# Optimization experiments

Measured on AMD Instinct MI355X. Metric: run time of the kernel, lower is better.

## Reference

```python
import jax, jax.numpy as jnp
import numpy as np

BATCH, T, N = 64, 512, 1024

def setup_inputs() -> dict:
    key = jax.random.key(0)
    k1, k2, k3 = jax.random.split(key, 3)
    input_sequence = jax.random.normal(k1, (BATCH, T, N), dtype=jnp.float32)
    W_self_lower = jax.random.normal(k2, (N, N), dtype=jnp.float32) * 0.1
    W_input = jax.random.normal(k3, (N, N), dtype=jnp.float32) * 0.1
    return {"input_sequence": input_sequence, "W_self_lower": W_self_lower, "W_input": W_input}

def reference(input_sequence, W_self_lower, W_input):
    # W_self symmetric: (W + W.T)/2; note W_self.T == W_self
    W_self = (W_self_lower + W_self_lower.T) * 0.5
    batch = input_sequence.shape[0]
    n = W_self.shape[0]
    # Precompute input projection for all timesteps: (B, T, N) @ (N, N)^T
    x_proj = jnp.einsum('btn,mn->btm', input_sequence, W_input)
    h0 = jnp.zeros((batch, n), dtype=input_sequence.dtype)

    def step(h, xp_t):
        h_new = jnp.tanh(h @ W_self.T + xp_t)
        return h_new, h_new

    # scan over time axis: move T to leading axis
    _, states = jax.lax.scan(step, h0, jnp.swapaxes(x_proj, 0, 1))
    return jnp.swapaxes(states, 0, 1)  # (B, T, N)
```

## Files before the change

### kernel.cpp

```cpp
#include <hip/hip_runtime.h>
#include <cstdint>
#include <cmath>

constexpr int BATCH = 64;
constexpr int T     = 512;
constexpr int N     = 1024;
constexpr int NWG   = 256;
constexpr int NG    = 32;
constexpr int GM    = 16;

typedef float f4 __attribute__((ext_vector_type(4)));
typedef short s4 __attribute__((ext_vector_type(4)));
typedef short bs8 __attribute__((ext_vector_type(8)));

struct alignas(128) PadInt { int v; int pad[31]; };
__device__ PadInt g_cnt[NG];
__device__ PadInt g_flag[NG];

__device__ __forceinline__ f4 ld_sys_x4(const float* p) {
  f4 v;
  asm volatile("global_load_dwordx4 %0, %1, off sc0 sc1" : "=v"(v) : "v"(p));
  return v;
}
__device__ __forceinline__ int ld_sys_i32(const int* p) {
  int v;
  asm volatile("global_load_dword %0, %1, off sc0 sc1\n\ts_waitcnt vmcnt(0)"
               : "=v"(v) : "v"(p) : "memory");
  return v;
}
__device__ __forceinline__ void st_sys_f32(float* p, float v) {
  asm volatile("global_store_dword %0, %1, off sc0 sc1 nt" ::"v"(p), "v"(v)
               : "memory");
}
__device__ __forceinline__ void wait_vm0(void) {
  asm volatile("s_waitcnt vmcnt(0)" ::: "memory");
  __builtin_amdgcn_sched_barrier(0);
}

__device__ __forceinline__ void arrive_cnt(int g, int t) {
  int old = __hip_atomic_fetch_add(&g_cnt[g].v, 1, __ATOMIC_RELAXED,
                                   __HIP_MEMORY_SCOPE_AGENT);
  if (old == t * GM + (GM - 1))
    __hip_atomic_store(&g_flag[g].v, t + 1, __ATOMIC_RELAXED,
                       __HIP_MEMORY_SCOPE_AGENT);
}
__device__ __forceinline__ void pollf(int g, int e) {
  while (ld_sys_i32(&g_flag[g].v) < e) __builtin_amdgcn_s_sleep(1);
}

__device__ __forceinline__ unsigned short f2bf(float f) {
  unsigned u = __builtin_bit_cast(unsigned, f);
  u = u + 0x7FFFu + ((u >> 16) & 1u);
  return (unsigned short)(u >> 16);
}
__device__ __forceinline__ float bf2f(unsigned short b) {
  unsigned u = ((unsigned)b) << 16;
  return __builtin_bit_cast(float, u);
}
__device__ __forceinline__ void mk8hilo(const float* p, bs8& hi, bs8& lo) {
  f4 a = *reinterpret_cast<const f4*>(p);
  f4 b = *reinterpret_cast<const f4*>(p + 4);
  float v[8] = {a[0], a[1], a[2], a[3], b[0], b[1], b[2], b[3]};
#pragma unroll
  for (int j = 0; j < 8; ++j) {
    unsigned short h = f2bf(v[j]);
    hi[j] = (short)h;
    lo[j] = (short)f2bf(v[j] - bf2f(h));
  }
}

__global__ __launch_bounds__(256) void symm_k(const float* __restrict__ W,
                                              float* __restrict__ Ws) {
  if (blockIdx.x == 0 && blockIdx.y == 0 && threadIdx.x < NG) {
    __hip_atomic_store(&g_cnt[threadIdx.x].v, 0, __ATOMIC_RELAXED,
                       __HIP_MEMORY_SCOPE_AGENT);
    __hip_atomic_store(&g_flag[threadIdx.x].v, 0, __ATOMIC_RELAXED,
                       __HIP_MEMORY_SCOPE_AGENT);
  }
  int j = blockIdx.x * 16 + (threadIdx.x & 15);
  int i = blockIdx.y * 16 + (threadIdx.x >> 4);
  Ws[(size_t)i * N + j] = 0.5f * (W[(size_t)i * N + j] + W[(size_t)j * N + i]);
}

__global__ __launch_bounds__(256) void xproj_gemm(const float* __restrict__ A,
                                                  const float* __restrict__ B,
                                                  float* __restrict__ C,
                                                  int M) {
  constexpr int BM = 128, BN = 128, BK = 16;
  __shared__ float As[BK][BM + 4];
  __shared__ float Bs[BK][BN + 4];

  const int tid = threadIdx.x;
  const int lin = blockIdx.x + gridDim.x * blockIdx.y;
  const int sw  = ((lin & 7) << 8) + (lin >> 3);
  const int bm  = sw >> 3;
  const int bn  = sw & 7;
  const int tx = tid & 15, ty = tid >> 4;
  const int K = N;

  float acc[8][8];
#pragma unroll
  for (int i = 0; i < 8; ++i)
#pragma unroll
    for (int j = 0; j < 8; ++j) acc[i][j] = 0.f;

  for (int kt = 0; kt < K; kt += BK) {
#pragma unroll
    for (int s = 0; s < 2; ++s) {
      int f = tid + s * 256;
      int row = f >> 2, kq = f & 3;
      float4 a = *reinterpret_cast<const float4*>(
          &A[(size_t)(bm * BM + row) * K + kt + kq * 4]);
      As[kq * 4 + 0][row] = a.x;
      As[kq * 4 + 1][row] = a.y;
      As[kq * 4 + 2][row] = a.z;
      As[kq * 4 + 3][row] = a.w;
      float4 b = *reinterpret_cast<const float4*>(
          &B[(size_t)(bn * BN + row) * K + kt + kq * 4]);
      Bs[kq * 4 + 0][row] = b.x;
      Bs[kq * 4 + 1][row] = b.y;
      Bs[kq * 4 + 2][row] = b.z;
      Bs[kq * 4 + 3][row] = b.w;
    }
    __syncthreads();

#pragma unroll
    for (int k = 0; k < BK; ++k) {
      float a[8], b[8];
      *reinterpret_cast<float4*>(&a[0]) =
          *reinterpret_cast<const float4*>(&As[k][ty * 8]);
      *reinterpret_cast<float4*>(&a[4]) =
          *reinterpret_cast<const float4*>(&As[k][ty * 8 + 4]);
      *reinterpret_cast<float4*>(&b[0]) =
          *reinterpret_cast<const float4*>(&Bs[k][tx * 8]);
      *reinterpret_cast<float4*>(&b[4]) =
          *reinterpret_cast<const float4*>(&Bs[k][tx * 8 + 4]);
#pragma unroll
      for (int i = 0; i < 8; ++i)
#pragma unroll
        for (int j = 0; j < 8; ++j) acc[i][j] = fmaf(a[i], b[j], acc[i][j]);
    }
    __syncthreads();
  }

#pragma unroll
  for (int i = 0; i < 8; ++i) {
    size_t row = (size_t)bm * BM + ty * 8 + i;
#pragma unroll
    for (int j = 0; j < 8; j += 4) {
      *reinterpret_cast<float4*>(&C[row * N + bn * BN + tx * 8 + j]) =
          *reinterpret_cast<const float4*>(&acc[i][j]);
    }
  }
}

__global__ __launch_bounds__(640, 1) void rnn_persist(
    float* __restrict__ out, const float* __restrict__ Ws) {
  const int tid = threadIdx.x;
  const int wg  = blockIdx.x;
  const int p   = wg & 15;
  const int cg  = wg >> 4;
  const int m0  = cg * 64;
  const int gA  = 2 * p, gB = 2 * p + 1;
  const int b0A = gA * 2, b0B = gB * 2;
  const size_t TN = (size_t)T * N;

  __shared__ __align__(16) short wloF[65536];
  __shared__ __align__(16) short hsA[4][1032];
  __shared__ __align__(16) short hsB[4][1032];
  __shared__ float xplA[128], xplB[128];
  __shared__ float redA[8 * 128], redB[8 * 128];
  __shared__ int lflags[64];

  if (tid == 0) {
    lflags[0] = -1; lflags[16] = -1;
    lflags[8] = 0;  lflags[24] = 0;
    lflags[32] = 0; lflags[48] = 0;
  }

  const int l = tid & 63;
  const int v = tid >> 6;
  const int n = l & 15;
  const int g = l >> 4;

  bs8 whi[4][4];
  if (v < 8) {
#pragma unroll
    for (int mt = 0; mt < 4; ++mt)
#pragma unroll
      for (int kt = 0; kt < 4; ++kt) {
        bs8 hi, lo;
        mk8hilo(&Ws[(size_t)(m0 + 16 * mt + n) * N + 128 * v + 32 * kt + 8 * g],
                hi, lo);
        whi[mt][kt] = hi;
        *reinterpret_cast<bs8*>(
            &wloF[((((v * 4 + mt) * 4 + kt) * 4 + g) * 16 + n) * 8]) = lo;
      }
  }
  __syncthreads();

  if (v < 8) {
    const int koff = 128 * v + 8 * g;
    const int hrow = n & 1;
    const int rcol = 8 * v + (l & 7);
    const int rnb  = (l >> 3) & 1;

    auto do_chain = [&](short (*hsX)[1032], float* xplX, float* redX,
                        int rdyIdx, int wsIdx, int ackIdx, int b0, int t) {
      while (*(volatile int*)&lflags[rdyIdx] < t) __builtin_amdgcn_s_sleep(1);
      __builtin_amdgcn_fence(__ATOMIC_ACQUIRE, "workgroup");
      if (t > 0) {
        f4 acc0 = {0.f, 0.f, 0.f, 0.f}, acc1 = {0.f, 0.f, 0.f, 0.f};
        f4 acc2 = {0.f, 0.f, 0.f, 0.f}, acc3 = {0.f, 0.f, 0.f, 0.f};
#pragma unroll
        for (int kt = 0; kt < 4; ++kt) {
          bs8 bhi = *reinterpret_cast<const bs8*>(&hsX[hrow][koff + 32 * kt]);
          bs8 blo = *reinterpret_cast<const bs8*>(&hsX[2 + hrow][koff + 32 * kt]);
          bs8 wl0 = *reinterpret_cast<const bs8*>(
              &wloF[((((v * 4 + 0) * 4 + kt) * 4 + g) * 16 + n) * 8]);
          bs8 wl1 = *reinterpret_cast<const bs8*>(
              &wloF[((((v * 4 + 1) * 4 + kt) * 4 + g) * 16 + n) * 8]);
          bs8 wl2 = *reinterpret_cast<const bs8*>(
              &wloF[((((v * 4 + 2) * 4 + kt) * 4 + g) * 16 + n) * 8]);
          bs8 wl3 = *reinterpret_cast<const bs8*>(
              &wloF[((((v * 4 + 3) * 4 + kt) * 4 + g) * 16 + n) * 8]);
          acc0 = __builtin_amdgcn_mfma_f32_16x16x32_bf16(whi[0][kt], bhi, acc0, 0, 0, 0);
          acc0 = __builtin_amdgcn_mfma_f32_16x16x32_bf16(whi[0][kt], blo, acc0, 0, 0, 0);
          acc0 = __builtin_amdgcn_mfma_f32_16x16x32_bf16(wl0, bhi, acc0, 0, 0, 0);
          acc1 = __builtin_amdgcn_mfma_f32_16x16x32_bf16(whi[1][kt], bhi, acc1, 0, 0, 0);
          acc1 = __builtin_amdgcn_mfma_f32_16x16x32_bf16(whi[1][kt], blo, acc1, 0, 0, 0);
          acc1 = __builtin_amdgcn_mfma_f32_16x16x32_bf16(wl1, bhi, acc1, 0, 0, 0);
          acc2 = __builtin_amdgcn_mfma_f32_16x16x32_bf16(whi[2][kt], bhi, acc2, 0, 0, 0);
          acc2 = __builtin_amdgcn_mfma_f32_16x16x32_bf16(whi[2][kt], blo, acc2, 0, 0, 0);
          acc2 = __builtin_amdgcn_mfma_f32_16x16x32_bf16(wl2, bhi, acc2, 0, 0, 0);
          acc3 = __builtin_amdgcn_mfma_f32_16x16x32_bf16(whi[3][kt], bhi, acc3, 0, 0, 0);
          acc3 = __builtin_amdgcn_mfma_f32_16x16x32_bf16(whi[3][kt], blo, acc3, 0, 0, 0);
          acc3 = __builtin_amdgcn_mfma_f32_16x16x32_bf16(wl3, bhi, acc3, 0, 0, 0);
        }
        if (n < 2) {
          const int rb = 4 * g;
#pragma unroll
          for (int r = 0; r < 4; ++r) {
            redX[v * 128 + (0  + rb + r) * 2 + n] = acc0[r];
            redX[v * 128 + (16 + rb + r) * 2 + n] = acc1[r];
            redX[v * 128 + (32 + rb + r) * 2 + n] = acc2[r];
            redX[v * 128 + (48 + rb + r) * 2 + n] = acc3[r];
          }
        }
      }
      __builtin_amdgcn_fence(__ATOMIC_RELEASE, "workgroup");
      if (l == 0) atomicAdd(&lflags[wsIdx], 1);
      while (*(volatile int*)&lflags[wsIdx] < 8 * (t + 1))
        __builtin_amdgcn_s_sleep(1);
      __builtin_amdgcn_fence(__ATOMIC_ACQUIRE, "workgroup");
      if (l < 16) {
        float pre = 0.f;
        if (t > 0) {
#pragma unroll
          for (int w = 0; w < 8; ++w)
            pre += redX[w * 128 + rcol * 2 + rnb];
        }
        float h = tanhf(pre + xplX[rnb * 64 + rcol]);
        st_sys_f32(out + (size_t)(b0 + rnb) * TN + (size_t)t * N + m0 + rcol,
                   h);
      }
      wait_vm0();
      if (l == 0) atomicAdd(&lflags[ackIdx], 1);
    };

    for (int t = 0; t < T; ++t) {
      do_chain(hsA, xplA, redA, 0, 8, 32, b0A, t);
      do_chain(hsB, xplB, redB, 16, 24, 48, b0B, t);
    }
  } else {
    const bool isB = (v == 9);
    const int lane = l;
    const int grp  = isB ? gB : gA;
    const int b0   = isB ? b0B : b0A;
    short (*hsb)[1032] = isB ? hsB : hsA;
    float* xpl = isB ? xplB : xplA;
    volatile int* ready = isB ? (volatile int*)&lflags[16]
                              : (volatile int*)&lflags[0];
    volatile int* cnt = isB ? (volatile int*)&lflags[48]
                            : (volatile int*)&lflags[32];

    const int r = lane >> 5;
    const int c = lane & 31;
    const float* hrow = out + (size_t)(b0 + r) * TN;
    const int xr = lane >> 4, xc = (lane & 15) * 4;
    const float* xsrc = out + (size_t)(b0 + xr) * TN + m0 + xc;

    f4 xnext;
    {
      f4 xv;
      if (lane < 32) xv = ld_sys_x4(xsrc);
      wait_vm0();
      if (lane < 32) *reinterpret_cast<f4*>(&xpl[xr * 64 + xc]) = xv;
      __builtin_amdgcn_fence(__ATOMIC_RELEASE, "workgroup");
      if (lane == 0) *ready = 0;
      if (lane < 32) xnext = ld_sys_x4(xsrc + (size_t)N);
    }

    for (int t = 1; t < T; ++t) {
      if (lane == 0) {
        while (*cnt < 8 * t) __builtin_amdgcn_s_sleep(1);
        arrive_cnt(grp, t - 1);
        pollf(grp, t);
      }
      const float* hs = hrow + (size_t)(t - 1) * N;
      f4 tmp[8];
#pragma unroll
      for (int q = 0; q < 8; ++q) tmp[q] = ld_sys_x4(hs + 4 * (c + 32 * q));
      wait_vm0();
#pragma unroll
      for (int q = 0; q < 8; ++q) {
        s4 hi4, lo4;
#pragma unroll
        for (int j = 0; j < 4; ++j) {
          float x = tmp[q][j];
          unsigned short h = f2bf(x);
          hi4[j] = (short)h;
          lo4[j] = (short)f2bf(x - bf2f(h));
        }
        *reinterpret_cast<s4*>(&hsb[r][4 * (c + 32 * q)]) = hi4;
        *reinterpret_cast<s4*>(&hsb[2 + r][4 * (c + 32 * q)]) = lo4;
      }
      if (lane < 32) *reinterpret_cast<f4*>(&xpl[xr * 64 + xc]) = xnext;
      __builtin_amdgcn_fence(__ATOMIC_RELEASE, "workgroup");
      if (lane == 0) *ready = t;
      if (t + 1 < T && lane < 32)
        xnext = ld_sys_x4(xsrc + (size_t)(t + 1) * N);
    }
  }
}

extern "C" void kernel_launch(void* const* d_in, const int* in_sizes, int n_in,
                              void* d_out, int out_size, void* d_ws,
                              size_t ws_size, hipStream_t stream) {
  const float* in_seq  = (const float*)d_in[0];
  const float* W_lower = (const float*)d_in[1];
  const float* W_input = (const float*)d_in[2];
  float* out = (float*)d_out;
  float* Ws  = (float*)d_ws;

  symm_k<<<dim3(N / 16, N / 16), 256, 0, stream>>>(W_lower, Ws);
  xproj_gemm<<<dim3(N / 128, (BATCH * T) / 128), 256, 0, stream>>>(
      in_seq, W_input, out, BATCH * T);
  rnn_persist<<<NWG, 640, 0, stream>>>(out, Ws);
}
```

Baseline: 2.780 ms.

## Split compute waves between the two batch chains instead of interleaving both per wave

Previously all 8 compute waves handled both chains A and B serially each timestep, each wave covering a 128-wide K slice. Now waves 0-3 serve chain A and waves 4-7 serve chain B, each covering a 256-wide K slice, so the two chains run concurrently rather than back to back. This is meant to let one chain's compute overlap the other's global sync latency. In exchange each wave does twice the K work per step and holds twice the hi weight fragments in registers, while the lo fragments in LDS are shared between the two wave groups.

```diff
diff --git a/kernel.cpp b/kernel.cpp
--- a/kernel.cpp
+++ b/kernel.cpp
@@ -169,7 +169,7 @@
   __shared__ __align__(16) short hsA[4][1032];
   __shared__ __align__(16) short hsB[4][1032];
   __shared__ float xplA[128], xplB[128];
-  __shared__ float redA[8 * 128], redB[8 * 128];
+  __shared__ float redA[4 * 128], redB[4 * 128];
   __shared__ int lflags[64];
 
   if (tid == 0) {
@@ -182,48 +182,60 @@
   const int v = tid >> 6;
   const int n = l & 15;
   const int g = l >> 4;
-
-  bs8 whi[4][4];
+  const int vl = v & 3;
+
+  bs8 whi[4][8];
   if (v < 8) {
 #pragma unroll
     for (int mt = 0; mt < 4; ++mt)
 #pragma unroll
-      for (int kt = 0; kt < 4; ++kt) {
+      for (int kt = 0; kt < 8; ++kt) {
         bs8 hi, lo;
-        mk8hilo(&Ws[(size_t)(m0 + 16 * mt + n) * N + 128 * v + 32 * kt + 8 * g],
-                hi, lo);
+        mk8hilo(
+            &Ws[(size_t)(m0 + 16 * mt + n) * N + 256 * vl + 32 * kt + 8 * g],
+            hi, lo);
         whi[mt][kt] = hi;
-        *reinterpret_cast<bs8*>(
-            &wloF[((((v * 4 + mt) * 4 + kt) * 4 + g) * 16 + n) * 8]) = lo;
+        if (v < 4)
+          *reinterpret_cast<bs8*>(
+              &wloF[((((vl * 4 + mt) * 8 + kt) * 4 + g) * 16 + n) * 8]) = lo;
       }
   }
   __syncthreads();
 
   if (v < 8) {
-    const int koff = 128 * v + 8 * g;
+    const bool isB = (v >= 4);
+    short (*hsX)[1032] = isB ? hsB : hsA;
+    float* xplX = isB ? xplB : xplA;
+    float* redX = isB ? redB : redA;
+    const int rdyIdx = isB ? 16 : 0;
+    const int wsIdx  = isB ? 24 : 8;
+    const int ackIdx = isB ? 48 : 32;
+    const int b0     = isB ? b0B : b0A;
+
+    const int koff = 256 * vl + 8 * g;
     const int hrow = n & 1;
-    const int rcol = 8 * v + (l & 7);
-    const int rnb  = (l >> 3) & 1;
-
-    auto do_chain = [&](short (*hsX)[1032], float* xplX, float* redX,
-                        int rdyIdx, int wsIdx, int ackIdx, int b0, int t) {
+    const int rcol = 16 * vl + (l & 15);
+    const int rnb  = (l >> 4) & 1;
+
+    for (int t = 0; t < T; ++t) {
       while (*(volatile int*)&lflags[rdyIdx] < t) __builtin_amdgcn_s_sleep(1);
       __builtin_amdgcn_fence(__ATOMIC_ACQUIRE, "workgroup");
       if (t > 0) {
         f4 acc0 = {0.f, 0.f, 0.f, 0.f}, acc1 = {0.f, 0.f, 0.f, 0.f};
         f4 acc2 = {0.f, 0.f, 0.f, 0.f}, acc3 = {0.f, 0.f, 0.f, 0.f};
 #pragma unroll
-        for (int kt = 0; kt < 4; ++kt) {
+        for (int kt = 0; kt < 8; ++kt) {
           bs8 bhi = *reinterpret_cast<const bs8*>(&hsX[hrow][koff + 32 * kt]);
-          bs8 blo = *reinterpret_cast<const bs8*>(&hsX[2 + hrow][koff + 32 * kt]);
+          bs8 blo =
+              *reinterpret_cast<const bs8*>(&hsX[2 + hrow][koff + 32 * kt]);
           bs8 wl0 = *reinterpret_cast<const bs8*>(
-              &wloF[((((v * 4 + 0) * 4 + kt) * 4 + g) * 16 + n) * 8]);
+              &wloF[((((vl * 4 + 0) * 8 + kt) * 4 + g) * 16 + n) * 8]);
           bs8 wl1 = *reinterpret_cast<const bs8*>(
-              &wloF[((((v * 4 + 1) * 4 + kt) * 4 + g) * 16 + n) * 8]);
+              &wloF[((((vl * 4 + 1) * 8 + kt) * 4 + g) * 16 + n) * 8]);
           bs8 wl2 = *reinterpret_cast<const bs8*>(
-              &wloF[((((v * 4 + 2) * 4 + kt) * 4 + g) * 16 + n) * 8]);
+              &wloF[((((vl * 4 + 2) * 8 + kt) * 4 + g) * 16 + n) * 8]);
           bs8 wl3 = *reinterpret_cast<const bs8*>(
-              &wloF[((((v * 4 + 3) * 4 + kt) * 4 + g) * 16 + n) * 8]);
+              &wloF[((((vl * 4 + 3) * 8 + kt) * 4 + g) * 16 + n) * 8]);
           acc0 = __builtin_amdgcn_mfma_f32_16x16x32_bf16(whi[0][kt], bhi, acc0, 0, 0, 0);
           acc0 = __builtin_amdgcn_mfma_f32_16x16x32_bf16(whi[0][kt], blo, acc0, 0, 0, 0);
           acc0 = __builtin_amdgcn_mfma_f32_16x16x32_bf16(wl0, bhi, acc0, 0, 0, 0);
@@ -241,23 +253,23 @@
           const int rb = 4 * g;
 #pragma unroll
           for (int r = 0; r < 4; ++r) {
-            redX[v * 128 + (0  + rb + r) * 2 + n] = acc0[r];
-            redX[v * 128 + (16 + rb + r) * 2 + n] = acc1[r];
-            redX[v * 128 + (32 + rb + r) * 2 + n] = acc2[r];
-            redX[v * 128 + (48 + rb + r) * 2 + n] = acc3[r];
+            redX[vl * 128 + (0  + rb + r) * 2 + n] = acc0[r];
+            redX[vl * 128 + (16 + rb + r) * 2 + n] = acc1[r];
+            redX[vl * 128 + (32 + rb + r) * 2 + n] = acc2[r];
+            redX[vl * 128 + (48 + rb + r) * 2 + n] = acc3[r];
           }
         }
       }
       __builtin_amdgcn_fence(__ATOMIC_RELEASE, "workgroup");
       if (l == 0) atomicAdd(&lflags[wsIdx], 1);
-      while (*(volatile int*)&lflags[wsIdx] < 8 * (t + 1))
+      while (*(volatile int*)&lflags[wsIdx] < 4 * (t + 1))
         __builtin_amdgcn_s_sleep(1);
       __builtin_amdgcn_fence(__ATOMIC_ACQUIRE, "workgroup");
-      if (l < 16) {
+      if (l < 32) {
         float pre = 0.f;
         if (t > 0) {
 #pragma unroll
-          for (int w = 0; w < 8; ++w)
+          for (int w = 0; w < 4; ++w)
             pre += redX[w * 128 + rcol * 2 + rnb];
         }
         float h = tanhf(pre + xplX[rnb * 64 + rcol]);
@@ -266,11 +278,6 @@
       }
       wait_vm0();
       if (l == 0) atomicAdd(&lflags[ackIdx], 1);
-    };
-
-    for (int t = 0; t < T; ++t) {
-      do_chain(hsA, xplA, redA, 0, 8, 32, b0A, t);
-      do_chain(hsB, xplB, redB, 16, 24, 48, b0B, t);
     }
   } else {
     const bool isB = (v == 9);
@@ -303,7 +310,7 @@
 
     for (int t = 1; t < T; ++t) {
       if (lane == 0) {
-        while (*cnt < 8 * t) __builtin_amdgcn_s_sleep(1);
+        while (*cnt < 4 * t) __builtin_amdgcn_s_sleep(1);
         arrive_cnt(grp, t - 1);
         pollf(grp, t);
       }
```

Result: slower. 3.289 ms (+18.3%).
